# Performance work log

Hardware: AMD Instinct MI355X
Metric: run time of the kernel (lower is better)

## Reference

```python
import jax, jax.numpy as jnp
import numpy as np

B, TI, TO = 32, 128, 64
VI, VO = 32000, 32000
E, H, A = 256, 512, 512
EOS, BOS = 0, 1


def setup_inputs() -> dict:
    key = jax.random.key(0)
    ks = jax.random.split(key, 24)
    def p(k, shape):
        return jax.random.normal(k, shape, jnp.float32) * 0.05
    return {
        "inp": jax.random.randint(ks[0], (B, TI), 0, VI),
        "out": jax.random.randint(ks[1], (B, TO), 0, VO),
        "emb_inp": p(ks[2], (VI, E)),
        "emb_out": p(ks[3], (VO, E)),
        "enc_Wih_f": p(ks[4], (3 * H, E)),
        "enc_Whh_f": p(ks[5], (3 * H, H)),
        "enc_bih_f": p(ks[6], (3 * H,)),
        "enc_bhh_f": p(ks[7], (3 * H,)),
        "enc_Wih_b": p(ks[8], (3 * H, E)),
        "enc_Whh_b": p(ks[9], (3 * H, H)),
        "enc_bih_b": p(ks[10], (3 * H,)),
        "enc_bhh_b": p(ks[11], (3 * H,)),
        "dec_start_W": p(ks[12], (H, 2 * H)),
        "dec_start_b": p(ks[13], (H,)),
        "dec_Wih": p(ks[14], (3 * H, E + 2 * H)),
        "dec_Whh": p(ks[15], (3 * H, H)),
        "dec_bih": p(ks[16], (3 * H,)),
        "dec_bhh": p(ks[17], (3 * H,)),
        "attn_Wenc": p(ks[18], (A, 2 * H)),
        "attn_benc": p(ks[19], (A,)),
        "attn_Wdec": p(ks[20], (A, H)),
        "attn_bdec": p(ks[21], (A,)),
        "attn_v": p(ks[22], (A,)),
        "attn_vb": jnp.zeros((), jnp.float32),
        "logits_W": p(ks[23], (VO, 3 * H)),
        "logits_b": jnp.zeros((VO,), jnp.float32),
    }


def _gru_dir(x, Wih, bih, Whh, bhh, reverse):
    # x: [B,T,E]; precompute input projections once: [B,T,3H]
    xp = jnp.einsum('bte,ge->btg', x, Wih) + bih
    Hd = Whh.shape[1]
    def step(h, xt):
        gh = h @ Whh.T + bhh
        xr, xz, xn = jnp.split(xt, 3, -1)
        hr, hz, hn = jnp.split(gh, 3, -1)
        r = jax.nn.sigmoid(xr + hr)
        z = jax.nn.sigmoid(xz + hz)
        n = jnp.tanh(xn + r * hn)
        h_new = (1.0 - z) * n + z * h
        return h_new, h_new
    h0 = jnp.zeros((x.shape[0], Hd), x.dtype)
    _, hs = jax.lax.scan(step, h0, jnp.swapaxes(xp, 0, 1), reverse=reverse)
    return jnp.swapaxes(hs, 0, 1)  # [B,T,H]


def _forward(inp, out, emb_inp, emb_out,
             enc_Wih_f, enc_Whh_f, enc_bih_f, enc_bhh_f,
             enc_Wih_b, enc_Whh_b, enc_bih_b, enc_bhh_b,
             dec_start_W, dec_start_b, dec_Wih, dec_Whh, dec_bih, dec_bhh,
             attn_Wenc, attn_benc, attn_Wdec, attn_bdec, attn_v, attn_vb,
             logits_W, logits_b):
    x = emb_inp[inp]  # [B,TI,E]
    ef = _gru_dir(x, enc_Wih_f, enc_bih_f, enc_Whh_f, enc_bhh_f, False)
    eb = _gru_dir(x, enc_Wih_b, enc_bih_b, enc_Whh_b, enc_bhh_b, True)
    enc = jnp.concatenate([ef, eb], -1)  # [B,TI,2H]
    mask = (inp != EOS).astype(jnp.float32)
    lengths = jnp.minimum(mask.sum(1).astype(jnp.int32), TI - 1)
    last = enc[jnp.arange(enc.shape[0]), lengths]  # [B,2H]
    dec0 = last @ dec_start_W.T + dec_start_b  # [B,H]
    enc_proj = jnp.einsum('btd,ad->bta', enc, attn_Wenc) + attn_benc  # [B,TI,A]

    def attend(dec):
        dp = dec @ attn_Wdec.T + attn_bdec  # [B,A]
        s = jnp.tanh(enc_proj + dp[:, None, :]) @ attn_v + attn_vb  # [B,TI]
        s = jnp.where(mask > 0, s, -jnp.inf)
        pr = jax.nn.softmax(s, -1)
        return jnp.einsum('bt,btd->bd', pr, enc), pr

    a0, _ = attend(dec0)

    def step(carry, tok):
        h, a = carry
        e = emb_out[tok]  # [B,E]
        xg = jnp.concatenate([e, a], -1) @ dec_Wih.T + dec_bih
        hg = h @ dec_Whh.T + dec_bhh
        xr, xz, xn = jnp.split(xg, 3, -1)
        hr, hz, hn = jnp.split(hg, 3, -1)
        r = jax.nn.sigmoid(xr + hr)
        z = jax.nn.sigmoid(xz + hz)
        n = jnp.tanh(xn + r * hn)
        h_new = (1.0 - z) * n + z * h
        a_new, _ = attend(h_new)
        lg = jnp.concatenate([h_new, a_new], -1) @ logits_W.T + logits_b
        return (h_new, a_new), lg

    toks = jnp.swapaxes(out[:, :-1], 0, 1)  # [TO-1, B]
    _, lgs = jax.lax.scan(step, (dec0, a0), toks)  # [TO-1,B,VO]
    first = jnp.log(jax.nn.one_hot(jnp.full((out.shape[0],), BOS), VO) + 1e-9)
    return jnp.swapaxes(jnp.concatenate([first[None], lgs], 0), 0, 1)  # [B,TO,VO]


def reference(inp, out, emb_inp, emb_out,
              enc_Wih_f, enc_Whh_f, enc_bih_f, enc_bhh_f,
              enc_Wih_b, enc_Whh_b, enc_bih_b, enc_bhh_b,
              dec_start_W, dec_start_b, dec_Wih, dec_Whh, dec_bih, dec_bhh,
              attn_Wenc, attn_benc, attn_Wdec, attn_bdec, attn_v, attn_vb,
              logits_W, logits_b):
    return _forward(inp, out, emb_inp, emb_out,
                    enc_Wih_f, enc_Whh_f, enc_bih_f, enc_bhh_f,
                    enc_Wih_b, enc_Whh_b, enc_bih_b, enc_bhh_b,
                    dec_start_W, dec_start_b, dec_Wih, dec_Whh, dec_bih, dec_bhh,
                    attn_Wenc, attn_benc, attn_Wdec, attn_bdec, attn_v, attn_vb,
                    logits_W, logits_b)
```

## Files before the change

### kernel.cpp

```cpp
#include <hip/hip_runtime.h>
#include <math.h>
#include <stdint.h>

#define B_   32
#define TI_  128
#define TO_  64
#define E_   256
#define H_   512
#define A_   512
#define VO_  32000
#define G3_  1536
#define D2H_ 1024

using short8 = __attribute__((ext_vector_type(8))) short;
using f32x4  = __attribute__((ext_vector_type(4))) float;
typedef __attribute__((ext_vector_type(2))) __bf16 bf16x2_t;

__device__ __forceinline__ unsigned short f2bf(float x) {
  uint32_t u = __builtin_bit_cast(uint32_t, x);
  uint32_t r = (u + 0x7fffu + ((u >> 16) & 1u)) >> 16;
  return (unsigned short)r;
}
__device__ __forceinline__ uint32_t pack2(float lo, float hi) {
  return (uint32_t)f2bf(lo) | ((uint32_t)f2bf(hi) << 16);
}
__device__ __forceinline__ float bflo(uint32_t u) { return __builtin_bit_cast(float, u << 16); }
__device__ __forceinline__ float bfhi(uint32_t u) { return __builtin_bit_cast(float, u & 0xffff0000u); }

#if __has_builtin(__builtin_amdgcn_fdot2_f32_bf16)
__device__ __forceinline__ float dot2bf(uint32_t a, uint32_t b, float c) {
  return __builtin_amdgcn_fdot2_f32_bf16(__builtin_bit_cast(bf16x2_t, a),
                                         __builtin_bit_cast(bf16x2_t, b), c, false);
}
#else
__device__ __forceinline__ float dot2bf(uint32_t a, uint32_t b, float c) {
  return fmaf(bfhi(a), bfhi(b), fmaf(bflo(a), bflo(b), c));
}
#endif

__device__ __forceinline__ float sigf(float x) {
  return __builtin_amdgcn_rcpf(1.f + __expf(-x));
}
__device__ __forceinline__ float tanhf_(float x) {
  return fmaf(-2.f, __builtin_amdgcn_rcpf(1.f + __expf(2.f * x)), 1.f);
}

__global__ __launch_bounds__(256) void k_init(unsigned short* __restrict__ tail) {
  int i = blockIdx.x * 256 + threadIdx.x;
  if (i < 32 * G3_) tail[i] = 0;
}

__global__ __launch_bounds__(256) void k_cvt_bf16(const float* __restrict__ in,
                                                  unsigned short* __restrict__ out, int n8) {
  int i = blockIdx.x * 256 + threadIdx.x;
  if (i >= n8) return;
  float4 a = ((const float4*)in)[2 * i];
  float4 b = ((const float4*)in)[2 * i + 1];
  uint4 o = { pack2(a.x, a.y), pack2(a.z, a.w), pack2(b.x, b.y), pack2(b.z, b.w) };
  ((uint4*)out)[i] = o;
}

__global__ __launch_bounds__(256) void k_cvt_multi(
    const float* __restrict__ i0, unsigned short* __restrict__ o0,
    const float* __restrict__ i1, unsigned short* __restrict__ o1,
    const float* __restrict__ i2, unsigned short* __restrict__ o2,
    const float* __restrict__ i3, unsigned short* __restrict__ o3,
    const float* __restrict__ i4, unsigned short* __restrict__ o4,
    const float* __restrict__ i5, unsigned short* __restrict__ o5,
    const float* __restrict__ i6, unsigned short* __restrict__ o6,
    const float* __restrict__ i7, unsigned short* __restrict__ o7) {
  int u = blockIdx.x * 256 + threadIdx.x;
  const float* in; unsigned short* out; int lu;
  if      (u < 98304)  { in = i0; out = o0; lu = u; }
  else if (u < 196608) { in = i1; out = o1; lu = u - 98304; }
  else if (u < 294912) { in = i2; out = o2; lu = u - 196608; }
  else if (u < 327680) { in = i3; out = o3; lu = u - 294912; }
  else if (u < 573440) { in = i4; out = o4; lu = u - 327680; }
  else if (u < 638976) { in = i5; out = o5; lu = u - 573440; }
  else if (u < 688128) { in = i6; out = o6; lu = u - 638976; }
  else if (u < 737280) { in = i7; out = o7; lu = u - 688128; }
  else return;
  float4 a = ((const float4*)in)[2 * lu];
  float4 b = ((const float4*)in)[2 * lu + 1];
  uint4 o = { pack2(a.x, a.y), pack2(a.z, a.w), pack2(b.x, b.y), pack2(b.z, b.w) };
  ((uint4*)out)[lu] = o;
}

__global__ __launch_bounds__(256) void k_gather_xb(const int* __restrict__ inp,
                                                   const float* __restrict__ emb,
                                                   unsigned short* __restrict__ xb) {
  int idx = blockIdx.x * 256 + threadIdx.x;
  if (idx >= 4096 * 32) return;
  int row = idx >> 5, e8 = idx & 31;
  int tok = inp[row];
  const float4* s = (const float4*)(emb + (size_t)tok * E_ + e8 * 8);
  float4 a = s[0], b = s[1];
  uint4 o = { pack2(a.x, a.y), pack2(a.z, a.w), pack2(b.x, b.y), pack2(b.z, b.w) };
  ((uint4*)xb)[idx] = o;
}

__global__ __launch_bounds__(256) void k_gather_xeb(const int* __restrict__ outi,
                                                    const float* __restrict__ emb,
                                                    unsigned short* __restrict__ xeb) {
  int idx = blockIdx.x * 256 + threadIdx.x;
  if (idx >= 2016 * 32) return;
  int row = idx >> 5, e8 = idx & 31;
  int i = row >> 5, b = row & 31;
  int tok = outi[b * TO_ + i];
  const float4* s = (const float4*)(emb + (size_t)tok * E_ + e8 * 8);
  float4 a = s[0], bb = s[1];
  uint4 o = { pack2(a.x, a.y), pack2(a.z, a.w), pack2(bb.x, bb.y), pack2(bb.z, bb.w) };
  ((uint4*)xeb)[idx] = o;
}

__global__ __launch_bounds__(256) void k_first(float* __restrict__ dout) {
  int idx = blockIdx.x * 256 + threadIdx.x;
  if (idx >= B_ * VO_) return;
  int b = idx / VO_, v = idx % VO_;
  dout[(size_t)b * TO_ * VO_ + v] = (v == 1) ? 0.f : -20.72326583694641f;
}

template <int MODE>
__global__ __launch_bounds__(256) void k_bgemm(
    const unsigned short* __restrict__ A, int lda,
    const unsigned short* __restrict__ Bt, int ldb,
    const float* __restrict__ bias,
    void* __restrict__ Cv, int ldc, int M, int N, int K) {
  __shared__ alignas(16) unsigned short As[128 * 32];
  __shared__ alignas(16) unsigned short Bs[128 * 32];
  const int tid = threadIdx.x;
  const int wave = tid >> 6, lane = tid & 63;
  const int m0 = blockIdx.y * 128, n0 = blockIdx.x * 128;
  const int wr = wave >> 1, wc = wave & 1;

  f32x4 acc[4][4];
#pragma unroll
  for (int i = 0; i < 4; ++i)
#pragma unroll
    for (int j = 0; j < 4; ++j) acc[i][j] = (f32x4){0.f, 0.f, 0.f, 0.f};

  const int srow = tid >> 2;
  const int sbyte = (tid & 3) * 16;
  const int fr = lane & 15;
  const int fkb = (lane >> 4) * 16;

  for (int k0 = 0; k0 < K; k0 += 32) {
#pragma unroll
    for (int rd = 0; rd < 2; ++rd) {
      int row = rd * 64 + srow;
      int ra = min(m0 + row, M - 1);
      const char* ga = (const char*)(A + (size_t)ra * lda + k0) + sbyte;
      const char* gb = (const char*)(Bt + (size_t)(n0 + row) * ldb + k0) + sbyte;
      __builtin_amdgcn_global_load_lds(
          (const __attribute__((address_space(1))) uint32_t*)ga,
          (__attribute__((address_space(3))) uint32_t*)((char*)As + rd * 4096 + wave * 1024),
          16, 0, 0);
      __builtin_amdgcn_global_load_lds(
          (const __attribute__((address_space(1))) uint32_t*)gb,
          (__attribute__((address_space(3))) uint32_t*)((char*)Bs + rd * 4096 + wave * 1024),
          16, 0, 0);
    }
    __syncthreads();

    short8 af[4], bf[4];
#pragma unroll
    for (int i = 0; i < 4; ++i) {
      int ar = wr * 64 + i * 16 + fr;
      int bc = wc * 64 + i * 16 + fr;
      af[i] = *(const short8*)((const char*)As + ar * 64 + fkb);
      bf[i] = *(const short8*)((const char*)Bs + bc * 64 + fkb);
    }
#pragma unroll
    for (int i = 0; i < 4; ++i)
#pragma unroll
      for (int j = 0; j < 4; ++j)
        acc[i][j] = __builtin_amdgcn_mfma_f32_16x16x32_bf16(af[i], bf[j], acc[i][j], 0, 0, 0);
    __syncthreads();
  }

  const int crow = (lane >> 4) * 4, ccol = lane & 15;
#pragma unroll
  for (int i = 0; i < 4; ++i) {
#pragma unroll
    for (int r = 0; r < 4; ++r) {
      int m = m0 + wr * 64 + i * 16 + crow + r;
      if (m >= M) continue;
#pragma unroll
      for (int j = 0; j < 4; ++j) {
        int n = n0 + wc * 64 + j * 16 + ccol;
        float v = acc[i][j][r] + (bias ? bias[n] : 0.f);
        if (MODE == 0) {
          ((float*)Cv)[(size_t)m * ldc + n] = v;
        } else if (MODE == 1) {
          ((unsigned short*)Cv)[(size_t)m * ldc + n] = f2bf(v);
        } else {
          int bb = m & 31, st = m >> 5;
          ((float*)Cv)[((size_t)bb * TO_ + st + 1) * VO_ + n] = v;
        }
      }
    }
  }
}

__global__ __launch_bounds__(256) void k_encoder(
    const unsigned short* __restrict__ xpb_f, const unsigned short* __restrict__ xpb_b,
    const unsigned short* __restrict__ Whhb_f, const float* __restrict__ bhh_f,
    const unsigned short* __restrict__ Whhb_b, const float* __restrict__ bhh_b,
    unsigned short* __restrict__ encb) {
  __shared__ alignas(16) float h[512];
  __shared__ uint32_t hb2[256];
  __shared__ uint32_t xrow[768];
  const int bid = blockIdx.x;
  const int dir = bid >> 5, b = bid & 31;
  const unsigned short* xpb = dir ? xpb_b : xpb_f;
  const unsigned short* Whh = dir ? Whhb_b : Whhb_f;
  const float* bhh = dir ? bhh_b : bhh_f;
  const int tid = threadIdx.x;
  const int c0 = 2 * tid, c1 = c0 + 1;

  h[c0] = 0.f; h[c1] = 0.f; hb2[tid] = 0u;
  const float br0 = bhh[c0], br1 = bhh[c1];
  const float bz0 = bhh[512 + c0], bz1 = bhh[512 + c1];
  const float bn0 = bhh[1024 + c0], bn1 = bhh[1024 + c1];
  const uint4* w_r0 = (const uint4*)(Whh + (size_t)c0 * 512);
  const uint4* w_r1 = (const uint4*)(Whh + (size_t)c1 * 512);
  const uint4* w_z0 = (const uint4*)(Whh + (size_t)(512 + c0) * 512);
  const uint4* w_z1 = (const uint4*)(Whh + (size_t)(512 + c1) * 512);
  const uint4* w_n0 = (const uint4*)(Whh + (size_t)(1024 + c0) * 512);
  const uint4* w_n1 = (const uint4*)(Whh + (size_t)(1024 + c1) * 512);

  for (int t = 0; t < TI_; ++t) {
    const int tt = dir ? (TI_ - 1 - t) : t;
    const uint32_t* xr = (const uint32_t*)(xpb + (size_t)(b * 128 + tt) * G3_);
    xrow[tid] = xr[tid];
    xrow[tid + 256] = xr[tid + 256];
    xrow[tid + 512] = xr[tid + 512];
    __syncthreads();

    float ar0 = 0.f, ar1 = 0.f, az0 = 0.f, az1 = 0.f, an0 = 0.f, an1 = 0.f;
#pragma unroll 4
    for (int k = 0; k < 64; ++k) {
      uint32_t p0 = hb2[4 * k], p1 = hb2[4 * k + 1], p2 = hb2[4 * k + 2], p3 = hb2[4 * k + 3];
      uint4 u;
      u = w_r0[k]; ar0 = dot2bf(p0, u.x, ar0); ar0 = dot2bf(p1, u.y, ar0);
                   ar0 = dot2bf(p2, u.z, ar0); ar0 = dot2bf(p3, u.w, ar0);
      u = w_r1[k]; ar1 = dot2bf(p0, u.x, ar1); ar1 = dot2bf(p1, u.y, ar1);
                   ar1 = dot2bf(p2, u.z, ar1); ar1 = dot2bf(p3, u.w, ar1);
      u = w_z0[k]; az0 = dot2bf(p0, u.x, az0); az0 = dot2bf(p1, u.y, az0);
                   az0 = dot2bf(p2, u.z, az0); az0 = dot2bf(p3, u.w, az0);
      u = w_z1[k]; az1 = dot2bf(p0, u.x, az1); az1 = dot2bf(p1, u.y, az1);
                   az1 = dot2bf(p2, u.z, az1); az1 = dot2bf(p3, u.w, az1);
      u = w_n0[k]; an0 = dot2bf(p0, u.x, an0); an0 = dot2bf(p1, u.y, an0);
                   an0 = dot2bf(p2, u.z, an0); an0 = dot2bf(p3, u.w, an0);
      u = w_n1[k]; an1 = dot2bf(p0, u.x, an1); an1 = dot2bf(p1, u.y, an1);
                   an1 = dot2bf(p2, u.z, an1); an1 = dot2bf(p3, u.w, an1);
    }
    uint32_t uxr = xrow[tid], uxz = xrow[256 + tid], uxn = xrow[512 + tid];
    float r0 = sigf(bflo(uxr) + ar0 + br0);
    float r1 = sigf(bfhi(uxr) + ar1 + br1);
    float z0 = sigf(bflo(uxz) + az0 + bz0);
    float z1 = sigf(bfhi(uxz) + az1 + bz1);
    float n0 = tanhf_(bflo(uxn) + r0 * (an0 + bn0));
    float n1 = tanhf_(bfhi(uxn) + r1 * (an1 + bn1));
    float hn0 = (1.f - z0) * n0 + z0 * h[c0];
    float hn1 = (1.f - z1) * n1 + z1 * h[c1];
    ((uint32_t*)encb)[(size_t)(b * 128 + tt) * 512 + dir * 256 + tid] = pack2(hn0, hn1);
    __syncthreads();
    h[c0] = hn0; h[c1] = hn1; hb2[tid] = pack2(hn0, hn1);
    __syncthreads();
  }
}

__global__ __launch_bounds__(256) void k_decoder(
    const int* __restrict__ inp,
    const unsigned short* __restrict__ encb,
    const unsigned short* __restrict__ encpb,
    const float* __restrict__ XE,
    const unsigned short* __restrict__ encWT,
    const float* __restrict__ dsW, const float* __restrict__ dsb,
    const unsigned short* __restrict__ dWhhb, const float* __restrict__ dbhh,
    const unsigned short* __restrict__ aWdecb, const float* __restrict__ abdec,
    const float* __restrict__ abenc,
    const float* __restrict__ av, const float* __restrict__ avb,
    unsigned short* __restrict__ HAb) {
  __shared__ alignas(16) uint32_t encp_s[128 * 257];
  __shared__ alignas(16) float h[512];
  __shared__ uint32_t hb2[256];
  __shared__ float pr[128];
  __shared__ uint32_t prb2[64];
  __shared__ float dp[512];
  __shared__ float red[256];
  __shared__ float msk[128];
  __shared__ alignas(16) float vstage[1024];
  const int b = blockIdx.x, tid = threadIdx.x;
  const int c0 = 2 * tid, c1 = c0 + 1;

  {
    const uint32_t* epg = (const uint32_t*)(encpb + (size_t)b * 128 * 512);
#pragma unroll 4
    for (int i = 0; i < 128; ++i) {
      int u = tid + i * 256;
      encp_s[(u >> 8) * 257 + (u & 255)] = epg[u];
    }
  }
  if (tid < 128) msk[tid] = (inp[b * TI_ + tid] != 0) ? 1.f : 0.f;
  __syncthreads();
  if (tid < 64) {
    float s = msk[tid] + msk[tid + 64];
#pragma unroll
    for (int off = 32; off > 0; off >>= 1) s += __shfl_xor(s, off);
    if (tid == 0) red[0] = s;
  }
  __syncthreads();
  const int len = min((int)red[0], TI_ - 1);

  {
    const uint32_t* lrow = (const uint32_t*)(encb + (size_t)(b * 128 + len) * D2H_);
    uint32_t u0 = lrow[tid], u1 = lrow[256 + tid];
    vstage[c0] = bflo(u0); vstage[c1] = bfhi(u0);
    vstage[512 + c0] = bflo(u1); vstage[512 + c1] = bfhi(u1);
    __syncthreads();
    const float4* w0 = (const float4*)(dsW + (size_t)c0 * D2H_);
    const float4* w1 = (const float4*)(dsW + (size_t)c1 * D2H_);
    float a0 = 0.f, a1 = 0.f;
#pragma unroll 4
    for (int k = 0; k < 256; ++k) {
      float4 l = *(const float4*)&vstage[4 * k];
      float4 q0 = w0[k], q1 = w1[k];
      a0 = fmaf(l.x, q0.x, fmaf(l.y, q0.y, fmaf(l.z, q0.z, fmaf(l.w, q0.w, a0))));
      a1 = fmaf(l.x, q1.x, fmaf(l.y, q1.y, fmaf(l.z, q1.z, fmaf(l.w, q1.w, a1))));
    }
    float h0v = a0 + dsb[c0], h1v = a1 + dsb[c1];
    __syncthreads();
    h[c0] = h0v; h[c1] = h1v; hb2[tid] = pack2(h0v, h1v);
    vstage[tid] = av[tid];
    vstage[256 + tid] = av[256 + tid];
    __syncthreads();
  }

  auto attend = [&](int step) {
    {
      const uint4* w0 = (const uint4*)(aWdecb + (size_t)c0 * 512);
      const uint4* w1 = (const uint4*)(aWdecb + (size_t)c1 * 512);
      float d0 = 0.f, d1 = 0.f;
#pragma unroll 8
      for (int k = 0; k < 64; ++k) {
        uint32_t p0 = hb2[4 * k], p1 = hb2[4 * k + 1], p2 = hb2[4 * k + 2], p3 = hb2[4 * k + 3];
        uint4 u0 = w0[k];
        d0 = dot2bf(p0, u0.x, d0); d0 = dot2bf(p1, u0.y, d0);
        d0 = dot2bf(p2, u0.z, d0); d0 = dot2bf(p3, u0.w, d0);
        uint4 u1 = w1[k];
        d1 = dot2bf(p0, u1.x, d1); d1 = dot2bf(p1, u1.y, d1);
        d1 = dot2bf(p2, u1.z, d1); d1 = dot2bf(p3, u1.w, d1);
      }
      dp[c0] = d0 + abdec[c0] + abenc[c0];
      dp[c1] = d1 + abdec[c1] + abenc[c1];
    }
    __syncthreads();
    {
      int t = tid & 127, half = tid >> 7;
      const uint32_t* ep = encp_s + t * 257 + half * 128;
      const float* dph = dp + half * 256;
      const float* vh = vstage + half * 256;
      float s = 0.f;
#pragma unroll 4
      for (int a2 = 0; a2 < 128; ++a2) {
        uint32_t u = ep[a2];
        s = fmaf(vh[2 * a2],     tanhf_(bflo(u) + dph[2 * a2]),     s);
        s = fmaf(vh[2 * a2 + 1], tanhf_(bfhi(u) + dph[2 * a2 + 1]), s);
      }
      red[tid] = s;
    }
    __syncthreads();
    if (tid < 128) {
      float s = red[tid] + red[tid + 128] + avb[0];
      red[tid] = (msk[tid] > 0.f) ? s : -1e30f;
    }
    __syncthreads();
    if (tid < 64) {
      float m = fmaxf(red[tid], red[tid + 64]);
#pragma unroll
      for (int off = 32; off > 0; off >>= 1) m = fmaxf(m, __shfl_xor(m, off));
      if (tid == 0) dp[0] = m;
    }
    __syncthreads();
    float mx = dp[0];
    if (tid < 128) red[tid] = __expf(red[tid] - mx);
    __syncthreads();
    if (tid < 64) {
      float s2 = red[tid] + red[tid + 64];
#pragma unroll
      for (int off = 32; off > 0; off >>= 1) s2 += __shfl_xor(s2, off);
      if (tid == 0) dp[1] = s2;
    }
    __syncthreads();
    float inv = __builtin_amdgcn_rcpf(dp[1]);
    if (tid < 128) pr[tid] = red[tid] * inv;
    __syncthreads();
    if (tid < 64) prb2[tid] = pack2(pr[2 * tid], pr[2 * tid + 1]);
    if (step >= 0) {
      const uint32_t* eb = (const uint32_t*)(encb + (size_t)b * 128 * D2H_);
      float x0 = 0.f, x1 = 0.f, x2 = 0.f, x3 = 0.f;
#pragma unroll 4
      for (int t = 0; t < 128; ++t) {
        float p = pr[t];
        uint32_t u0 = eb[(size_t)t * 512 + tid];
        uint32_t u1 = eb[(size_t)t * 512 + 256 + tid];
        x0 = fmaf(p, bflo(u0), x0); x1 = fmaf(p, bfhi(u0), x1);
        x2 = fmaf(p, bflo(u1), x2); x3 = fmaf(p, bfhi(u1), x3);
      }
      uint32_t* hrow = (uint32_t*)(HAb + ((size_t)step * 32 + b) * G3_);
      hrow[256 + tid] = pack2(x0, x1);
      hrow[512 + tid] = pack2(x2, x3);
    }
    __syncthreads();
  };

  auto gru = [&](int i) {
    float xa[6], ha[6];
#pragma unroll
    for (int g = 0; g < 3; ++g) {
      const uint4* e0 = (const uint4*)(encWT + (size_t)(g * 512 + c0) * 4096 + b * 128);
      const uint4* e1 = (const uint4*)(encWT + (size_t)(g * 512 + c1) * 4096 + b * 128);
      float s0 = 0.f, s1 = 0.f;
#pragma unroll
      for (int k = 0; k < 16; ++k) {
        uint32_t p0 = prb2[4 * k], p1 = prb2[4 * k + 1], p2 = prb2[4 * k + 2], p3 = prb2[4 * k + 3];
        uint4 u0 = e0[k];
        s0 = dot2bf(p0, u0.x, s0); s0 = dot2bf(p1, u0.y, s0);
        s0 = dot2bf(p2, u0.z, s0); s0 = dot2bf(p3, u0.w, s0);
        uint4 u1 = e1[k];
        s1 = dot2bf(p0, u1.x, s1); s1 = dot2bf(p1, u1.y, s1);
        s1 = dot2bf(p2, u1.z, s1); s1 = dot2bf(p3, u1.w, s1);
      }
      xa[g * 2] = s0; xa[g * 2 + 1] = s1;
    }
#pragma unroll
    for (int g = 0; g < 3; ++g) {
      const uint4* w0 = (const uint4*)(dWhhb + (size_t)(g * 512 + c0) * 512);
      const uint4* w1 = (const uint4*)(dWhhb + (size_t)(g * 512 + c1) * 512);
      float s0 = 0.f, s1 = 0.f;
#pragma unroll 8
      for (int k = 0; k < 64; ++k) {
        uint32_t p0 = hb2[4 * k], p1 = hb2[4 * k + 1], p2 = hb2[4 * k + 2], p3 = hb2[4 * k + 3];
        uint4 u0 = w0[k];
        s0 = dot2bf(p0, u0.x, s0); s0 = dot2bf(p1, u0.y, s0);
        s0 = dot2bf(p2, u0.z, s0); s0 = dot2bf(p3, u0.w, s0);
        uint4 u1 = w1[k];
        s1 = dot2bf(p0, u1.x, s1); s1 = dot2bf(p1, u1.y, s1);
        s1 = dot2bf(p2, u1.z, s1); s1 = dot2bf(p3, u1.w, s1);
      }
      ha[g * 2] = s0; ha[g * 2 + 1] = s1;
    }
    const float* xrow = XE + ((size_t)i * 32 + b) * G3_;
    float r0 = sigf(xrow[c0] + xa[0] + ha[0] + dbhh[c0]);
    float r1 = sigf(xrow[c1] + xa[1] + ha[1] + dbhh[c1]);
    float z0 = sigf(xrow[512 + c0] + xa[2] + ha[2] + dbhh[512 + c0]);
    float z1 = sigf(xrow[512 + c1] + xa[3] + ha[3] + dbhh[512 + c1]);
    float n0 = tanhf_(xrow[1024 + c0] + xa[4] + r0 * (ha[4] + dbhh[1024 + c0]));
    float n1 = tanhf_(xrow[1024 + c1] + xa[5] + r1 * (ha[5] + dbhh[1024 + c1]));
    float hn0 = (1.f - z0) * n0 + z0 * h[c0];
    float hn1 = (1.f - z1) * n1 + z1 * h[c1];
    ((uint32_t*)(HAb + ((size_t)i * 32 + b) * G3_))[tid] = pack2(hn0, hn1);
    __syncthreads();
    h[c0] = hn0; h[c1] = hn1; hb2[tid] = pack2(hn0, hn1);
    __syncthreads();
  };

  attend(-1);
  for (int i = 0; i < 63; ++i) {
    gru(i);
    attend(i);
  }
}


extern "C" void kernel_launch(void* const* d_in, const int* in_sizes, int n_in,
                              void* d_out, int out_size, void* d_ws, size_t ws_size,
                              hipStream_t stream) {
  const int*   inp     = (const int*)d_in[0];
  const int*   outi    = (const int*)d_in[1];
  const float* emb_inp = (const float*)d_in[2];
  const float* emb_out = (const float*)d_in[3];
  const float* eWih_f  = (const float*)d_in[4];
  const float* eWhh_f  = (const float*)d_in[5];
  const float* ebih_f  = (const float*)d_in[6];
  const float* ebhh_f  = (const float*)d_in[7];
  const float* eWih_b  = (const float*)d_in[8];
  const float* eWhh_b  = (const float*)d_in[9];
  const float* ebih_b  = (const float*)d_in[10];
  const float* ebhh_b  = (const float*)d_in[11];
  const float* dsW     = (const float*)d_in[12];
  const float* dsb     = (const float*)d_in[13];
  const float* dWih    = (const float*)d_in[14];
  const float* dWhh    = (const float*)d_in[15];
  const float* dbih    = (const float*)d_in[16];
  const float* dbhh    = (const float*)d_in[17];
  const float* aWenc   = (const float*)d_in[18];
  const float* abenc   = (const float*)d_in[19];
  const float* aWdec   = (const float*)d_in[20];
  const float* abdec   = (const float*)d_in[21];
  const float* av      = (const float*)d_in[22];
  const float* avb     = (const float*)d_in[23];
  const float* lW      = (const float*)d_in[24];
  const float* lb      = (const float*)d_in[25];
  float* dout = (float*)d_out;

  char* ws = (char*)d_ws;
  size_t off = 0;
  auto alloc = [&](size_t bytes) {
    void* p = ws + off;
    off += (bytes + 255) & ~(size_t)255;
    return p;
  };
  unsigned short* xb      = (unsigned short*)alloc((size_t)4096 * 256 * 2);
  unsigned short* xeb     = (unsigned short*)alloc((size_t)2016 * 256 * 2);
  unsigned short* xpb_f   = (unsigned short*)alloc((size_t)4096 * G3_ * 2);
  unsigned short* xpb_b   = (unsigned short*)alloc((size_t)4096 * G3_ * 2);
  unsigned short* encb    = (unsigned short*)alloc((size_t)4096 * D2H_ * 2);
  unsigned short* encpb   = (unsigned short*)alloc((size_t)4096 * 512 * 2);
  unsigned short* encWT   = (unsigned short*)alloc((size_t)G3_ * 4096 * 2);
  float*          XE      = (float*)alloc((size_t)2016 * G3_ * 4);
  unsigned short* HAb     = (unsigned short*)alloc((size_t)2048 * G3_ * 2);
  unsigned short* lWb     = (unsigned short*)alloc((size_t)VO_ * G3_ * 2);
  unsigned short* eWhhb_f = (unsigned short*)alloc((size_t)G3_ * 512 * 2);
  unsigned short* eWhhb_b = (unsigned short*)alloc((size_t)G3_ * 512 * 2);
  unsigned short* dWhhb   = (unsigned short*)alloc((size_t)G3_ * 512 * 2);
  unsigned short* aWdecb  = (unsigned short*)alloc((size_t)512 * 512 * 2);
  unsigned short* dWihb   = (unsigned short*)alloc((size_t)G3_ * 1280 * 2);
  unsigned short* aWencb  = (unsigned short*)alloc((size_t)512 * D2H_ * 2);
  unsigned short* eWihb_f = (unsigned short*)alloc((size_t)G3_ * 256 * 2);
  unsigned short* eWihb_b = (unsigned short*)alloc((size_t)G3_ * 256 * 2);

  k_init<<<192, 256, 0, stream>>>(HAb + (size_t)2016 * G3_);
  k_cvt_multi<<<2880, 256, 0, stream>>>(eWhh_f, eWhhb_f, eWhh_b, eWhhb_b,
                                        dWhh, dWhhb, aWdec, aWdecb,
                                        dWih, dWihb, aWenc, aWencb,
                                        eWih_f, eWihb_f, eWih_b, eWihb_b);
  k_cvt_bf16<<<24000, 256, 0, stream>>>(lW, lWb, VO_ * G3_ / 8);

  k_gather_xb<<<512, 256, 0, stream>>>(inp, emb_inp, xb);
  k_gather_xeb<<<252, 256, 0, stream>>>(outi, emb_out, xeb);

  {
    dim3 g(12, 32);
    k_bgemm<1><<<g, 256, 0, stream>>>(xb, 256, eWihb_f, 256, ebih_f, xpb_f, G3_, 4096, G3_, 256);
    k_bgemm<1><<<g, 256, 0, stream>>>(xb, 256, eWihb_b, 256, ebih_b, xpb_b, G3_, 4096, G3_, 256);
  }

  k_encoder<<<64, 256, 0, stream>>>(xpb_f, xpb_b, eWhhb_f, ebhh_f, eWhhb_b, ebhh_b, encb);

  {
    dim3 g(4, 32);
    k_bgemm<1><<<g, 256, 0, stream>>>(encb, D2H_, aWencb, D2H_, nullptr, encpb, 512, 4096, 512, D2H_);
  }
  {
    dim3 g(32, 12);
    k_bgemm<1><<<g, 256, 0, stream>>>(dWihb + 256, 1280, encb, D2H_, nullptr, encWT, 4096, G3_, 4096, D2H_);
  }
  {
    dim3 g(12, 16);
    k_bgemm<0><<<g, 256, 0, stream>>>(xeb, 256, dWihb, 1280, dbih, XE, G3_, 2016, G3_, 256);
  }

  k_decoder<<<32, 256, 0, stream>>>(inp, encb, encpb, XE, encWT, dsW, dsb,
                                    dWhhb, dbhh, aWdecb, abdec, abenc, av, avb, HAb);

  {
    dim3 g(250, 16);
    k_bgemm<3><<<g, 256, 0, stream>>>(HAb, G3_, lWb, G3_, lb, dout, 0, 2016, VO_, G3_);
  }
  k_first<<<4000, 256, 0, stream>>>(dout);
}
```

Before: 12.00 ms.

## Use k-pair-major transposed weights and 1024-thread blocks in recurrent kernels

Pre-transposes the recurrent weight matrices (encoder Whh, decoder Whh, attention Wdec, and the per-batch attention-projected encoder states) into a k-pair-major layout, so adjacent threads read adjacent columns with coalesced 32-bit loads. The encoder and decoder recurrences now run with 1024 threads per block, two threads per output column splitting the k range and combining through a shuffle. The decoder no longer stages encpb in shared memory and reads it from global instead. The aim is to cut per-step latency in the serial recurrences by raising parallelism and memory coalescing, at the cost of extra transpose kernels and more synchronisation per step.

```diff
diff --git a/kernel.cpp b/kernel.cpp
--- a/kernel.cpp
+++ b/kernel.cpp
@@ -64,26 +64,45 @@
     const float* __restrict__ i0, unsigned short* __restrict__ o0,
     const float* __restrict__ i1, unsigned short* __restrict__ o1,
     const float* __restrict__ i2, unsigned short* __restrict__ o2,
-    const float* __restrict__ i3, unsigned short* __restrict__ o3,
-    const float* __restrict__ i4, unsigned short* __restrict__ o4,
-    const float* __restrict__ i5, unsigned short* __restrict__ o5,
-    const float* __restrict__ i6, unsigned short* __restrict__ o6,
-    const float* __restrict__ i7, unsigned short* __restrict__ o7) {
+    const float* __restrict__ i3, unsigned short* __restrict__ o3) {
   int u = blockIdx.x * 256 + threadIdx.x;
   const float* in; unsigned short* out; int lu;
-  if      (u < 98304)  { in = i0; out = o0; lu = u; }
-  else if (u < 196608) { in = i1; out = o1; lu = u - 98304; }
-  else if (u < 294912) { in = i2; out = o2; lu = u - 196608; }
-  else if (u < 327680) { in = i3; out = o3; lu = u - 294912; }
-  else if (u < 573440) { in = i4; out = o4; lu = u - 327680; }
-  else if (u < 638976) { in = i5; out = o5; lu = u - 573440; }
-  else if (u < 688128) { in = i6; out = o6; lu = u - 638976; }
-  else if (u < 737280) { in = i7; out = o7; lu = u - 688128; }
+  if      (u < 245760) { in = i0; out = o0; lu = u; }
+  else if (u < 311296) { in = i1; out = o1; lu = u - 245760; }
+  else if (u < 360448) { in = i2; out = o2; lu = u - 311296; }
+  else if (u < 409600) { in = i3; out = o3; lu = u - 360448; }
   else return;
   float4 a = ((const float4*)in)[2 * lu];
   float4 b = ((const float4*)in)[2 * lu + 1];
   uint4 o = { pack2(a.x, a.y), pack2(a.z, a.w), pack2(b.x, b.y), pack2(b.z, b.w) };
   ((uint4*)out)[lu] = o;
+}
+
+__global__ __launch_bounds__(256) void k_cvt_tp(
+    const float* __restrict__ i0, uint32_t* __restrict__ o0,
+    const float* __restrict__ i1, uint32_t* __restrict__ o1,
+    const float* __restrict__ i2, uint32_t* __restrict__ o2,
+    const float* __restrict__ i3, uint32_t* __restrict__ o3) {
+  int u = blockIdx.x * 256 + threadIdx.x;
+  const float* in; uint32_t* out; int lu, N;
+  if      (u < 393216)  { in = i0; out = o0; lu = u;          N = 1536; }
+  else if (u < 786432)  { in = i1; out = o1; lu = u - 393216; N = 1536; }
+  else if (u < 1179648) { in = i2; out = o2; lu = u - 786432; N = 1536; }
+  else if (u < 1310720) { in = i3; out = o3; lu = u - 1179648; N = 512; }
+  else return;
+  int c = lu % N, kp = lu / N;
+  const float* p = in + (size_t)c * 512 + 2 * kp;
+  out[lu] = pack2(p[0], p[1]);
+}
+
+__global__ __launch_bounds__(256) void k_packT(const unsigned short* __restrict__ encWA,
+                                               uint32_t* __restrict__ EWPd) {
+  int idx = blockIdx.x * 256 + threadIdx.x;
+  if (idx >= 32 * 64 * 1536) return;
+  int g = idx % 1536, q = idx / 1536;
+  int b = q >> 6, tp = q & 63;
+  size_t r0 = ((size_t)(b * 128 + 2 * tp)) * 1536 + g;
+  EWPd[idx] = (uint32_t)encWA[r0] | ((uint32_t)encWA[r0 + 1536] << 16);
 }
 
 __global__ __launch_bounds__(256) void k_gather_xb(const int* __restrict__ inp,
@@ -202,268 +221,261 @@
   }
 }
 
-__global__ __launch_bounds__(256) void k_encoder(
+__global__ __launch_bounds__(1024, 4) void k_encoder(
     const unsigned short* __restrict__ xpb_f, const unsigned short* __restrict__ xpb_b,
-    const unsigned short* __restrict__ Whhb_f, const float* __restrict__ bhh_f,
-    const unsigned short* __restrict__ Whhb_b, const float* __restrict__ bhh_b,
+    const uint32_t* __restrict__ EWPf, const float* __restrict__ bhh_f,
+    const uint32_t* __restrict__ EWPb, const float* __restrict__ bhh_b,
     unsigned short* __restrict__ encb) {
-  __shared__ alignas(16) float h[512];
+  __shared__ uint32_t xrow[768];
+  __shared__ float hf[512];
   __shared__ uint32_t hb2[256];
-  __shared__ uint32_t xrow[768];
   const int bid = blockIdx.x;
   const int dir = bid >> 5, b = bid & 31;
   const unsigned short* xpb = dir ? xpb_b : xpb_f;
-  const unsigned short* Whh = dir ? Whhb_b : Whhb_f;
+  const uint32_t* EWP = dir ? EWPb : EWPf;
   const float* bhh = dir ? bhh_b : bhh_f;
   const int tid = threadIdx.x;
-  const int c0 = 2 * tid, c1 = c0 + 1;
-
-  h[c0] = 0.f; h[c1] = 0.f; hb2[tid] = 0u;
-  const float br0 = bhh[c0], br1 = bhh[c1];
-  const float bz0 = bhh[512 + c0], bz1 = bhh[512 + c1];
-  const float bn0 = bhh[1024 + c0], bn1 = bhh[1024 + c1];
-  const uint4* w_r0 = (const uint4*)(Whh + (size_t)c0 * 512);
-  const uint4* w_r1 = (const uint4*)(Whh + (size_t)c1 * 512);
-  const uint4* w_z0 = (const uint4*)(Whh + (size_t)(512 + c0) * 512);
-  const uint4* w_z1 = (const uint4*)(Whh + (size_t)(512 + c1) * 512);
-  const uint4* w_n0 = (const uint4*)(Whh + (size_t)(1024 + c0) * 512);
-  const uint4* w_n1 = (const uint4*)(Whh + (size_t)(1024 + c1) * 512);
+  const int col = tid >> 1, kh = tid & 1;
+
+  if (tid < 512) hf[tid] = 0.f;
+  if (tid < 256) hb2[tid] = 0u;
+  float br = 0.f, bz = 0.f, bn = 0.f;
+  if (kh == 0) { br = bhh[col]; bz = bhh[512 + col]; bn = bhh[1024 + col]; }
+  uint32_t* encw = (uint32_t*)encb;
 
   for (int t = 0; t < TI_; ++t) {
     const int tt = dir ? (TI_ - 1 - t) : t;
     const uint32_t* xr = (const uint32_t*)(xpb + (size_t)(b * 128 + tt) * G3_);
-    xrow[tid] = xr[tid];
-    xrow[tid + 256] = xr[tid + 256];
-    xrow[tid + 512] = xr[tid + 512];
-    __syncthreads();
-
-    float ar0 = 0.f, ar1 = 0.f, az0 = 0.f, az1 = 0.f, an0 = 0.f, an1 = 0.f;
-#pragma unroll 4
-    for (int k = 0; k < 64; ++k) {
-      uint32_t p0 = hb2[4 * k], p1 = hb2[4 * k + 1], p2 = hb2[4 * k + 2], p3 = hb2[4 * k + 3];
-      uint4 u;
-      u = w_r0[k]; ar0 = dot2bf(p0, u.x, ar0); ar0 = dot2bf(p1, u.y, ar0);
-                   ar0 = dot2bf(p2, u.z, ar0); ar0 = dot2bf(p3, u.w, ar0);
-      u = w_r1[k]; ar1 = dot2bf(p0, u.x, ar1); ar1 = dot2bf(p1, u.y, ar1);
-                   ar1 = dot2bf(p2, u.z, ar1); ar1 = dot2bf(p3, u.w, ar1);
-      u = w_z0[k]; az0 = dot2bf(p0, u.x, az0); az0 = dot2bf(p1, u.y, az0);
-                   az0 = dot2bf(p2, u.z, az0); az0 = dot2bf(p3, u.w, az0);
-      u = w_z1[k]; az1 = dot2bf(p0, u.x, az1); az1 = dot2bf(p1, u.y, az1);
-                   az1 = dot2bf(p2, u.z, az1); az1 = dot2bf(p3, u.w, az1);
-      u = w_n0[k]; an0 = dot2bf(p0, u.x, an0); an0 = dot2bf(p1, u.y, an0);
-                   an0 = dot2bf(p2, u.z, an0); an0 = dot2bf(p3, u.w, an0);
-      u = w_n1[k]; an1 = dot2bf(p0, u.x, an1); an1 = dot2bf(p1, u.y, an1);
-                   an1 = dot2bf(p2, u.z, an1); an1 = dot2bf(p3, u.w, an1);
-    }
-    uint32_t uxr = xrow[tid], uxz = xrow[256 + tid], uxn = xrow[512 + tid];
-    float r0 = sigf(bflo(uxr) + ar0 + br0);
-    float r1 = sigf(bfhi(uxr) + ar1 + br1);
-    float z0 = sigf(bflo(uxz) + az0 + bz0);
-    float z1 = sigf(bfhi(uxz) + az1 + bz1);
-    float n0 = tanhf_(bflo(uxn) + r0 * (an0 + bn0));
-    float n1 = tanhf_(bfhi(uxn) + r1 * (an1 + bn1));
-    float hn0 = (1.f - z0) * n0 + z0 * h[c0];
-    float hn1 = (1.f - z1) * n1 + z1 * h[c1];
-    ((uint32_t*)encb)[(size_t)(b * 128 + tt) * 512 + dir * 256 + tid] = pack2(hn0, hn1);
-    __syncthreads();
-    h[c0] = hn0; h[c1] = hn1; hb2[tid] = pack2(hn0, hn1);
-    __syncthreads();
-  }
-}
-
-__global__ __launch_bounds__(256) void k_decoder(
+    if (tid < 768) xrow[tid] = xr[tid];
+    __syncthreads();
+
+    float ar = 0.f, az = 0.f, an = 0.f;
+    const uint32_t* wp = EWP + (size_t)(kh * 128) * 1536 + col;
+#pragma unroll 8
+    for (int k = 0; k < 128; ++k) {
+      uint32_t hv = hb2[kh * 128 + k];
+      ar = dot2bf(hv, wp[0], ar);
+      az = dot2bf(hv, wp[512], az);
+      an = dot2bf(hv, wp[1024], an);
+      wp += 1536;
+    }
+    ar += __shfl_xor(ar, 1);
+    az += __shfl_xor(az, 1);
+    an += __shfl_xor(an, 1);
+
+    float hnew = 0.f;
+    if (kh == 0) {
+      uint32_t ur = xrow[col >> 1], uz = xrow[256 + (col >> 1)], un = xrow[512 + (col >> 1)];
+      float xrv = (col & 1) ? bfhi(ur) : bflo(ur);
+      float xzv = (col & 1) ? bfhi(uz) : bflo(uz);
+      float xnv = (col & 1) ? bfhi(un) : bflo(un);
+      float r = sigf(xrv + ar + br);
+      float z = sigf(xzv + az + bz);
+      float n = tanhf_(xnv + r * (an + bn));
+      hnew = (1.f - z) * n + z * hf[col];
+    }
+    __syncthreads();
+    float hnb = __shfl_down(hnew, 2);
+    if ((tid & 3) == 0)
+      encw[(size_t)(b * 128 + tt) * 512 + dir * 256 + (tid >> 2)] = pack2(hnew, hnb);
+    if (kh == 0) hf[col] = hnew;
+    __syncthreads();
+    if (tid < 256) hb2[tid] = pack2(hf[2 * tid], hf[2 * tid + 1]);
+    __syncthreads();
+  }
+}
+
+__global__ __launch_bounds__(1024, 4) void k_decoder(
     const int* __restrict__ inp,
     const unsigned short* __restrict__ encb,
     const unsigned short* __restrict__ encpb,
     const float* __restrict__ XE,
-    const unsigned short* __restrict__ encWT,
+    const uint32_t* __restrict__ EWPd,
+    const uint32_t* __restrict__ WHPd,
+    const uint32_t* __restrict__ WDPd,
     const float* __restrict__ dsW, const float* __restrict__ dsb,
-    const unsigned short* __restrict__ dWhhb, const float* __restrict__ dbhh,
-    const unsigned short* __restrict__ aWdecb, const float* __restrict__ abdec,
-    const float* __restrict__ abenc,
+    const float* __restrict__ dbhh,
+    const float* __restrict__ abdec, const float* __restrict__ abenc,
     const float* __restrict__ av, const float* __restrict__ avb,
     unsigned short* __restrict__ HAb) {
-  __shared__ alignas(16) uint32_t encp_s[128 * 257];
-  __shared__ alignas(16) float h[512];
+  __shared__ float hf[512];
   __shared__ uint32_t hb2[256];
+  __shared__ uint32_t prb2[64];
   __shared__ float pr[128];
-  __shared__ uint32_t prb2[64];
+  __shared__ float sc[128];
+  __shared__ float msk[128];
   __shared__ float dp[512];
-  __shared__ float red[256];
-  __shared__ float msk[128];
-  __shared__ alignas(16) float vstage[1024];
+  __shared__ float vavf[512];
+  __shared__ float red[1024];
+  __shared__ float red2[1024];
+  __shared__ float dpx[4];
   const int b = blockIdx.x, tid = threadIdx.x;
-  const int c0 = 2 * tid, c1 = c0 + 1;
-
-  {
-    const uint32_t* epg = (const uint32_t*)(encpb + (size_t)b * 128 * 512);
-#pragma unroll 4
-    for (int i = 0; i < 128; ++i) {
-      int u = tid + i * 256;
-      encp_s[(u >> 8) * 257 + (u & 255)] = epg[u];
-    }
-  }
+  const int col = tid >> 1, kh = tid & 1;
+
+  float db_r = 0.f, db_z = 0.f, db_n = 0.f, adb = 0.f;
+  if (kh == 0) {
+    db_r = dbhh[col]; db_z = dbhh[512 + col]; db_n = dbhh[1024 + col];
+    adb = abdec[col] + abenc[col];
+  }
+  const float avb0 = avb[0];
+
   if (tid < 128) msk[tid] = (inp[b * TI_ + tid] != 0) ? 1.f : 0.f;
+  if (tid < 512) vavf[tid] = av[tid];
   __syncthreads();
   if (tid < 64) {
     float s = msk[tid] + msk[tid + 64];
 #pragma unroll
-    for (int off = 32; off > 0; off >>= 1) s += __shfl_xor(s, off);
-    if (tid == 0) red[0] = s;
+    for (int o = 32; o > 0; o >>= 1) s += __shfl_xor(s, o);
+    if (tid == 0) dpx[0] = s;
   }
   __syncthreads();
-  const int len = min((int)red[0], TI_ - 1);
-
+  const int len = min((int)dpx[0], TI_ - 1);
+
+  if (tid < 512) {
+    uint32_t u = ((const uint32_t*)encb)[(size_t)(b * 128 + len) * 512 + tid];
+    red[2 * tid] = bflo(u);
+    red[2 * tid + 1] = bfhi(u);
+  }
+  __syncthreads();
   {
-    const uint32_t* lrow = (const uint32_t*)(encb + (size_t)(b * 128 + len) * D2H_);
-    uint32_t u0 = lrow[tid], u1 = lrow[256 + tid];
-    vstage[c0] = bflo(u0); vstage[c1] = bfhi(u0);
-    vstage[512 + c0] = bflo(u1); vstage[512 + c1] = bfhi(u1);
-    __syncthreads();
-    const float4* w0 = (const float4*)(dsW + (size_t)c0 * D2H_);
-    const float4* w1 = (const float4*)(dsW + (size_t)c1 * D2H_);
-    float a0 = 0.f, a1 = 0.f;
-#pragma unroll 4
-    for (int k = 0; k < 256; ++k) {
-      float4 l = *(const float4*)&vstage[4 * k];
-      float4 q0 = w0[k], q1 = w1[k];
-      a0 = fmaf(l.x, q0.x, fmaf(l.y, q0.y, fmaf(l.z, q0.z, fmaf(l.w, q0.w, a0))));
-      a1 = fmaf(l.x, q1.x, fmaf(l.y, q1.y, fmaf(l.z, q1.z, fmaf(l.w, q1.w, a1))));
-    }
-    float h0v = a0 + dsb[c0], h1v = a1 + dsb[c1];
-    __syncthreads();
-    h[c0] = h0v; h[c1] = h1v; hb2[tid] = pack2(h0v, h1v);
-    vstage[tid] = av[tid];
-    vstage[256 + tid] = av[256 + tid];
+    const float4* w = (const float4*)(dsW + (size_t)col * D2H_ + kh * 512);
+    float acc = 0.f;
+#pragma unroll 8
+    for (int k = 0; k < 128; ++k) {
+      float4 l = ((const float4*)red)[kh * 128 + k];
+      float4 q = w[k];
+      acc = fmaf(l.x, q.x, fmaf(l.y, q.y, fmaf(l.z, q.z, fmaf(l.w, q.w, acc))));
+    }
+    acc += __shfl_xor(acc, 1);
+    __syncthreads();
+    if (kh == 0) hf[col] = acc + dsb[col];
+    __syncthreads();
+    if (tid < 256) hb2[tid] = pack2(hf[2 * tid], hf[2 * tid + 1]);
     __syncthreads();
   }
 
   auto attend = [&](int step) {
     {
-      const uint4* w0 = (const uint4*)(aWdecb + (size_t)c0 * 512);
-      const uint4* w1 = (const uint4*)(aWdecb + (size_t)c1 * 512);
-      float d0 = 0.f, d1 = 0.f;
+      const uint32_t* wp = WDPd + (size_t)(kh * 128) * 512 + col;
+      float d_ = 0.f;
 #pragma unroll 8
-      for (int k = 0; k < 64; ++k) {
-        uint32_t p0 = hb2[4 * k], p1 = hb2[4 * k + 1], p2 = hb2[4 * k + 2], p3 = hb2[4 * k + 3];
-        uint4 u0 = w0[k];
-        d0 = dot2bf(p0, u0.x, d0); d0 = dot2bf(p1, u0.y, d0);
-        d0 = dot2bf(p2, u0.z, d0); d0 = dot2bf(p3, u0.w, d0);
-        uint4 u1 = w1[k];
-        d1 = dot2bf(p0, u1.x, d1); d1 = dot2bf(p1, u1.y, d1);
-        d1 = dot2bf(p2, u1.z, d1); d1 = dot2bf(p3, u1.w, d1);
-      }
-      dp[c0] = d0 + abdec[c0] + abenc[c0];
-      dp[c1] = d1 + abdec[c1] + abenc[c1];
+      for (int k = 0; k < 128; ++k) {
+        d_ = dot2bf(hb2[kh * 128 + k], wp[0], d_);
+        wp += 512;
+      }
+      d_ += __shfl_xor(d_, 1);
+      if (kh == 0) dp[col] = d_ + adb;
     }
     __syncthreads();
     {
-      int t = tid & 127, half = tid >> 7;
-      const uint32_t* ep = encp_s + t * 257 + half * 128;
-      const float* dph = dp + half * 256;
-      const float* vh = vstage + half * 256;
+      int t = tid >> 3, s8 = tid & 7;
+      const uint32_t* ep = (const uint32_t*)encpb + (size_t)(b * 128 + t) * 256 + s8;
       float s = 0.f;
 #pragma unroll 4
-      for (int a2 = 0; a2 < 128; ++a2) {
-        uint32_t u = ep[a2];
-        s = fmaf(vh[2 * a2],     tanhf_(bflo(u) + dph[2 * a2]),     s);
-        s = fmaf(vh[2 * a2 + 1], tanhf_(bfhi(u) + dph[2 * a2 + 1]), s);
-      }
-      red[tid] = s;
-    }
-    __syncthreads();
-    if (tid < 128) {
-      float s = red[tid] + red[tid + 128] + avb[0];
-      red[tid] = (msk[tid] > 0.f) ? s : -1e30f;
-    }
+      for (int i = 0; i < 32; ++i) {
+        int j = s8 + 8 * i;
+        uint32_t u = ep[8 * i];
+        float2 d2 = *(const float2*)&dp[2 * j];
+        float2 v2 = *(const float2*)&vavf[2 * j];
+        s = fmaf(v2.x, tanhf_(bflo(u) + d2.x), s);
+        s = fmaf(v2.y, tanhf_(bfhi(u) + d2.y), s);
+      }
+      s += __shfl_xor(s, 1);
+      s += __shfl_xor(s, 2);
+      s += __shfl_xor(s, 4);
+      if (s8 == 0) sc[t] = s;
+    }
+    __syncthreads();
+    if (tid < 128) sc[tid] = (msk[tid] > 0.f) ? sc[tid] + avb0 : -1e30f;
     __syncthreads();
     if (tid < 64) {
-      float m = fmaxf(red[tid], red[tid + 64]);
-#pragma unroll
-      for (int off = 32; off > 0; off >>= 1) m = fmaxf(m, __shfl_xor(m, off));
-      if (tid == 0) dp[0] = m;
-    }
-    __syncthreads();
-    float mx = dp[0];
-    if (tid < 128) red[tid] = __expf(red[tid] - mx);
+      float m = fmaxf(sc[tid], sc[tid + 64]);
+#pragma unroll
+      for (int o = 32; o > 0; o >>= 1) m = fmaxf(m, __shfl_xor(m, o));
+      if (tid == 0) dpx[1] = m;
+    }
+    __syncthreads();
+    if (tid < 128) pr[tid] = __expf(sc[tid] - dpx[1]);
     __syncthreads();
     if (tid < 64) {
-      float s2 = red[tid] + red[tid + 64];
-#pragma unroll
-      for (int off = 32; off > 0; off >>= 1) s2 += __shfl_xor(s2, off);
-      if (tid == 0) dp[1] = s2;
-    }
-    __syncthreads();
-    float inv = __builtin_amdgcn_rcpf(dp[1]);
-    if (tid < 128) pr[tid] = red[tid] * inv;
+      float s2 = pr[tid] + pr[tid + 64];
+#pragma unroll
+      for (int o = 32; o > 0; o >>= 1) s2 += __shfl_xor(s2, o);
+      if (tid == 0) dpx[2] = s2;
+    }
+    __syncthreads();
+    float inv = __builtin_amdgcn_rcpf(dpx[2]);
+    if (tid < 128) pr[tid] *= inv;
     __syncthreads();
     if (tid < 64) prb2[tid] = pack2(pr[2 * tid], pr[2 * tid + 1]);
     if (step >= 0) {
-      const uint32_t* eb = (const uint32_t*)(encb + (size_t)b * 128 * D2H_);
-      float x0 = 0.f, x1 = 0.f, x2 = 0.f, x3 = 0.f;
+      const uint32_t* eb = (const uint32_t*)encb + (size_t)b * 128 * 512;
+      int d = tid & 511, tq = tid >> 9;
+      float x0 = 0.f, x1 = 0.f;
 #pragma unroll 4
-      for (int t = 0; t < 128; ++t) {
+      for (int k = 0; k < 64; ++k) {
+        int t = tq * 64 + k;
         float p = pr[t];
-        uint32_t u0 = eb[(size_t)t * 512 + tid];
-        uint32_t u1 = eb[(size_t)t * 512 + 256 + tid];
-        x0 = fmaf(p, bflo(u0), x0); x1 = fmaf(p, bfhi(u0), x1);
-        x2 = fmaf(p, bflo(u1), x2); x3 = fmaf(p, bfhi(u1), x3);
-      }
-      uint32_t* hrow = (uint32_t*)(HAb + ((size_t)step * 32 + b) * G3_);
-      hrow[256 + tid] = pack2(x0, x1);
-      hrow[512 + tid] = pack2(x2, x3);
+        uint32_t u = eb[(size_t)t * 512 + d];
+        x0 = fmaf(p, bflo(u), x0);
+        x1 = fmaf(p, bfhi(u), x1);
+      }
+      red[tid] = x0; red2[tid] = x1;
+      __syncthreads();
+      if (tid < 512) {
+        x0 = red[tid] + red[tid + 512];
+        x1 = red2[tid] + red2[tid + 512];
+        uint32_t* hrow = (uint32_t*)(HAb + ((size_t)step * 32 + b) * G3_);
+        hrow[256 + tid] = pack2(x0, x1);
+      }
     }
     __syncthreads();
   };
 
   auto gru = [&](int i) {
-    float xa[6], ha[6];
-#pragma unroll
-    for (int g = 0; g < 3; ++g) {
-      const uint4* e0 = (const uint4*)(encWT + (size_t)(g * 512 + c0) * 4096 + b * 128);
-      const uint4* e1 = (const uint4*)(encWT + (size_t)(g * 512 + c1) * 4096 + b * 128);
-      float s0 = 0.f, s1 = 0.f;
-#pragma unroll
-      for (int k = 0; k < 16; ++k) {
-        uint32_t p0 = prb2[4 * k], p1 = prb2[4 * k + 1], p2 = prb2[4 * k + 2], p3 = prb2[4 * k + 3];
-        uint4 u0 = e0[k];
-        s0 = dot2bf(p0, u0.x, s0); s0 = dot2bf(p1, u0.y, s0);
-        s0 = dot2bf(p2, u0.z, s0); s0 = dot2bf(p3, u0.w, s0);
-        uint4 u1 = e1[k];
-        s1 = dot2bf(p0, u1.x, s1); s1 = dot2bf(p1, u1.y, s1);
-        s1 = dot2bf(p2, u1.z, s1); s1 = dot2bf(p3, u1.w, s1);
-      }
-      xa[g * 2] = s0; xa[g * 2 + 1] = s1;
-    }
-#pragma unroll
-    for (int g = 0; g < 3; ++g) {
-      const uint4* w0 = (const uint4*)(dWhhb + (size_t)(g * 512 + c0) * 512);
-      const uint4* w1 = (const uint4*)(dWhhb + (size_t)(g * 512 + c1) * 512);
-      float s0 = 0.f, s1 = 0.f;
+    float xr_ = 0.f, xz_ = 0.f, xn_ = 0.f, hr_ = 0.f, hz_ = 0.f, hn_ = 0.f;
+    {
+      const uint32_t* ew = EWPd + ((size_t)b * 64 + kh * 32) * 1536 + col;
 #pragma unroll 8
-      for (int k = 0; k < 64; ++k) {
-        uint32_t p0 = hb2[4 * k], p1 = hb2[4 * k + 1], p2 = hb2[4 * k + 2], p3 = hb2[4 * k + 3];
-        uint4 u0 = w0[k];
-        s0 = dot2bf(p0, u0.x, s0); s0 = dot2bf(p1, u0.y, s0);
-        s0 = dot2bf(p2, u0.z, s0); s0 = dot2bf(p3, u0.w, s0);
-        uint4 u1 = w1[k];
-        s1 = dot2bf(p0, u1.x, s1); s1 = dot2bf(p1, u1.y, s1);
-        s1 = dot2bf(p2, u1.z, s1); s1 = dot2bf(p3, u1.w, s1);
-      }
-      ha[g * 2] = s0; ha[g * 2 + 1] = s1;
-    }
-    const float* xrow = XE + ((size_t)i * 32 + b) * G3_;
-    float r0 = sigf(xrow[c0] + xa[0] + ha[0] + dbhh[c0]);
-    float r1 = sigf(xrow[c1] + xa[1] + ha[1] + dbhh[c1]);
-    float z0 = sigf(xrow[512 + c0] + xa[2] + ha[2] + dbhh[512 + c0]);
-    float z1 = sigf(xrow[512 + c1] + xa[3] + ha[3] + dbhh[512 + c1]);
-    float n0 = tanhf_(xrow[1024 + c0] + xa[4] + r0 * (ha[4] + dbhh[1024 + c0]));
-    float n1 = tanhf_(xrow[1024 + c1] + xa[5] + r1 * (ha[5] + dbhh[1024 + c1]));
-    float hn0 = (1.f - z0) * n0 + z0 * h[c0];
-    float hn1 = (1.f - z1) * n1 + z1 * h[c1];
-    ((uint32_t*)(HAb + ((size_t)i * 32 + b) * G3_))[tid] = pack2(hn0, hn1);
-    __syncthreads();
-    h[c0] = hn0; h[c1] = hn1; hb2[tid] = pack2(hn0, hn1);
+      for (int k = 0; k < 32; ++k) {
+        uint32_t pv = prb2[kh * 32 + k];
+        xr_ = dot2bf(pv, ew[0], xr_);
+        xz_ = dot2bf(pv, ew[512], xz_);
+        xn_ = dot2bf(pv, ew[1024], xn_);
+        ew += 1536;
+      }
+    }
+    {
+      const uint32_t* wp = WHPd + (size_t)(kh * 128) * 1536 + col;
+#pragma unroll 8
+      for (int k = 0; k < 128; ++k) {
+        uint32_t hv = hb2[kh * 128 + k];
+        hr_ = dot2bf(hv, wp[0], hr_);
+        hz_ = dot2bf(hv, wp[512], hz_);
+        hn_ = dot2bf(hv, wp[1024], hn_);
+        wp += 1536;
+      }
+    }
+    float t_r = xr_ + hr_; t_r += __shfl_xor(t_r, 1);
+    float t_z = xz_ + hz_; t_z += __shfl_xor(t_z, 1);
+    xn_ += __shfl_xor(xn_, 1);
+    hn_ += __shfl_xor(hn_, 1);
+
+    float hnew = 0.f;
+    if (kh == 0) {
+      const float* xrow = XE + ((size_t)i * 32 + b) * G3_;
+      float r = sigf(xrow[col] + t_r + db_r);
+      float z = sigf(xrow[512 + col] + t_z + db_z);
+      float n = tanhf_(xrow[1024 + col] + xn_ + r * (hn_ + db_n));
+      hnew = (1.f - z) * n + z * hf[col];
+    }
+    __syncthreads();
+    float hnb = __shfl_down(hnew, 2);
+    if ((tid & 3) == 0)
+      ((uint32_t*)(HAb + ((size_t)i * 32 + b) * G3_))[tid >> 2] = pack2(hnew, hnb);
+    if (kh == 0) hf[col] = hnew;
+    __syncthreads();
+    if (tid < 256) hb2[tid] = pack2(hf[2 * tid], hf[2 * tid + 1]);
     __syncthreads();
   };
 
@@ -519,24 +531,24 @@
   unsigned short* xpb_b   = (unsigned short*)alloc((size_t)4096 * G3_ * 2);
   unsigned short* encb    = (unsigned short*)alloc((size_t)4096 * D2H_ * 2);
   unsigned short* encpb   = (unsigned short*)alloc((size_t)4096 * 512 * 2);
-  unsigned short* encWT   = (unsigned short*)alloc((size_t)G3_ * 4096 * 2);
+  unsigned short* encWA   = (unsigned short*)alloc((size_t)4096 * G3_ * 2);
+  uint32_t*       EWPd    = (uint32_t*)alloc((size_t)32 * 64 * 1536 * 4);
   float*          XE      = (float*)alloc((size_t)2016 * G3_ * 4);
   unsigned short* HAb     = (unsigned short*)alloc((size_t)2048 * G3_ * 2);
   unsigned short* lWb     = (unsigned short*)alloc((size_t)VO_ * G3_ * 2);
-  unsigned short* eWhhb_f = (unsigned short*)alloc((size_t)G3_ * 512 * 2);
-  unsigned short* eWhhb_b = (unsigned short*)alloc((size_t)G3_ * 512 * 2);
-  unsigned short* dWhhb   = (unsigned short*)alloc((size_t)G3_ * 512 * 2);
-  unsigned short* aWdecb  = (unsigned short*)alloc((size_t)512 * 512 * 2);
+  uint32_t*       EWPf    = (uint32_t*)alloc((size_t)256 * 1536 * 4);
+  uint32_t*       EWPb    = (uint32_t*)alloc((size_t)256 * 1536 * 4);
+  uint32_t*       WHPd    = (uint32_t*)alloc((size_t)256 * 1536 * 4);
+  uint32_t*       WDPd    = (uint32_t*)alloc((size_t)256 * 512 * 4);
   unsigned short* dWihb   = (unsigned short*)alloc((size_t)G3_ * 1280 * 2);
   unsigned short* aWencb  = (unsigned short*)alloc((size_t)512 * D2H_ * 2);
   unsigned short* eWihb_f = (unsigned short*)alloc((size_t)G3_ * 256 * 2);
   unsigned short* eWihb_b = (unsigned short*)alloc((size_t)G3_ * 256 * 2);
 
   k_init<<<192, 256, 0, stream>>>(HAb + (size_t)2016 * G3_);
-  k_cvt_multi<<<2880, 256, 0, stream>>>(eWhh_f, eWhhb_f, eWhh_b, eWhhb_b,
-                                        dWhh, dWhhb, aWdec, aWdecb,
-                                        dWih, dWihb, aWenc, aWencb,
+  k_cvt_multi<<<1600, 256, 0, stream>>>(dWih, dWihb, aWenc, aWencb,
                                         eWih_f, eWihb_f, eWih_b, eWihb_b);
+  k_cvt_tp<<<5120, 256, 0, stream>>>(eWhh_f, EWPf, eWhh_b, EWPb, dWhh, WHPd, aWdec, WDPd);
   k_cvt_bf16<<<24000, 256, 0, stream>>>(lW, lWb, VO_ * G3_ / 8);
 
   k_gather_xb<<<512, 256, 0, stream>>>(inp, emb_inp, xb);
@@ -548,23 +560,25 @@
     k_bgemm<1><<<g, 256, 0, stream>>>(xb, 256, eWihb_b, 256, ebih_b, xpb_b, G3_, 4096, G3_, 256);
   }
 
-  k_encoder<<<64, 256, 0, stream>>>(xpb_f, xpb_b, eWhhb_f, ebhh_f, eWhhb_b, ebhh_b, encb);
+  k_encoder<<<64, 1024, 0, stream>>>(xpb_f, xpb_b, EWPf, ebhh_f, EWPb, ebhh_b, encb);
 
   {
     dim3 g(4, 32);
     k_bgemm<1><<<g, 256, 0, stream>>>(encb, D2H_, aWencb, D2H_, nullptr, encpb, 512, 4096, 512, D2H_);
   }
   {
-    dim3 g(32, 12);
-    k_bgemm<1><<<g, 256, 0, stream>>>(dWihb + 256, 1280, encb, D2H_, nullptr, encWT, 4096, G3_, 4096, D2H_);
-  }
+    dim3 g(12, 32);
+    k_bgemm<1><<<g, 256, 0, stream>>>(encb, D2H_, dWihb + 256, 1280, nullptr, encWA, G3_, 4096, G3_, D2H_);
+  }
+  k_packT<<<12288, 256, 0, stream>>>(encWA, EWPd);
+
   {
     dim3 g(12, 16);
     k_bgemm<0><<<g, 256, 0, stream>>>(xeb, 256, dWihb, 1280, dbih, XE, G3_, 2016, G3_, 256);
   }
 
-  k_decoder<<<32, 256, 0, stream>>>(inp, encb, encpb, XE, encWT, dsW, dsb,
-                                    dWhhb, dbhh, aWdecb, abdec, abenc, av, avb, HAb);
+  k_decoder<<<32, 1024, 0, stream>>>(inp, encb, encpb, XE, EWPd, WHPd, WDPd,
+                                     dsW, dsb, dbhh, abdec, abenc, av, avb, HAb);
 
   {
     dim3 g(250, 16);
```

Measured after the change: 11.10 ms. 1.08x faster.
